# Performance work log

Measured on AMD Instinct MI355X. Metric: run time of the kernel, lower is better.

## Reference

```python
import jax, jax.numpy as jnp
import numpy as np
from jax import lax

B, C, H, W = 8, 64, 256, 256
LENGTH = 9
REDUCTION = 8
HIDDEN = max(8, C // REDUCTION)


def _conv(x, w, b, pad):
    # x: [B,Cin,H,W], w: [Cout,Cin,kh,kw]
    y = lax.conv_general_dilated(x, w, (1, 1), [(pad, pad), (pad, pad)],
                                 dimension_numbers=('NCHW', 'OIHW', 'NCHW'))
    return y + b[None, :, None, None]


def _bilinear(img, cy, cx):
    # img: [B,C,H,W]; cy,cx: [B,H,W] float coords already clipped to [0, size-1]
    # Matches F.grid_sample(mode='bilinear', padding_mode='border', align_corners=True)
    Hh, Ww = img.shape[2], img.shape[3]
    y0 = jnp.floor(cy)
    x0 = jnp.floor(cx)
    wy = (cy - y0)[:, None]  # [B,1,H,W]
    wx = (cx - x0)[:, None]
    y0i = y0.astype(jnp.int32)
    x0i = x0.astype(jnp.int32)
    y1i = jnp.minimum(y0i + 1, Hh - 1)
    x1i = jnp.minimum(x0i + 1, Ww - 1)

    def g(im, iy, ix):
        return im[:, iy, ix]  # [C,H,W]

    gather = jax.vmap(g)
    v00 = gather(img, y0i, x0i)
    v01 = gather(img, y0i, x1i)
    v10 = gather(img, y1i, x0i)
    v11 = gather(img, y1i, x1i)
    return (v00 * (1 - wy) * (1 - wx) + v01 * (1 - wy) * wx
            + v10 * wy * (1 - wx) + v11 * wy * wx)


def _oriented_pool(x, vx, vy, length):
    # x: [B,C,H,W]; vx,vy: [B,1,H,W] direction fields
    _, _, Hh, Ww = x.shape
    yy = jnp.arange(Hh, dtype=x.dtype)[None, :, None]  # [1,H,1]
    xx = jnp.arange(Ww, dtype=x.dtype)[None, None, :]  # [1,1,W]
    half = length // 2
    offsets = jnp.arange(-half, half + 1, dtype=x.dtype)
    vx2 = vx[:, 0]  # [B,H,W]
    vy2 = vy[:, 0]

    def step(acc, t):
        cy = jnp.clip(yy + t * vy2, 0.0, Hh - 1)
        cx = jnp.clip(xx + t * vx2, 0.0, Ww - 1)
        return acc + _bilinear(x, cy, cx), None

    acc, _ = lax.scan(step, jnp.zeros_like(x), offsets)
    return acc / length


def setup_inputs() -> dict:
    key = jax.random.key(0)
    ks = jax.random.split(key, 5)

    def he(k, shape, fan_in):
        return jax.random.normal(k, shape, jnp.float32) * np.float32(1.0 / np.sqrt(fan_in))

    return {
        'x': jax.random.normal(ks[0], (B, C, H, W), jnp.float32),
        'w3': he(ks[1], (HIDDEN, C, 3, 3), C * 9),
        'b3': jnp.zeros((HIDDEN,), jnp.float32),
        'w1': he(ks[2], (1, HIDDEN, 1, 1), HIDDEN),
        'b1': jnp.zeros((1,), jnp.float32),
        'wr': he(ks[3], (HIDDEN, 2 * C, 1, 1), 2 * C),
        'br': jnp.zeros((HIDDEN,), jnp.float32),
        'we': he(ks[4], (2 * C, HIDDEN, 1, 1), HIDDEN),
        'be': jnp.zeros((2 * C,), jnp.float32),
    }


def reference(x, w3, b3, w1, b1, wr, br, we, be):
    theta = jnp.pi * jax.nn.sigmoid(_conv(jax.nn.relu(_conv(x, w3, b3, 1)), w1, b1, 0))  # [B,1,H,W]
    cos_t = jnp.cos(theta)
    sin_t = jnp.sin(theta)
    tan_feat = _oriented_pool(x, cos_t, sin_t, LENGTH)
    nor_feat = _oriented_pool(x, -sin_t, cos_t, LENGTH)
    context = jnp.concatenate([tan_feat, nor_feat], axis=1)  # [B,2C,H,W]
    w = jax.nn.sigmoid(_conv(jax.nn.relu(_conv(context, wr, br, 0)), we, be, 0))  # [B,2C,H,W]
    alpha_tan, alpha_norm = jnp.split(w, 2, axis=1)
    return (alpha_tan + alpha_norm) * x
```

## Files before the change

### kernel.cpp

```cpp
#include <hip/hip_runtime.h>
#include <math.h>

#define Bb 8
#define Cc 64
#define Hh 256
#define Ww 256
#define HID 8
#define PLANE (Hh*Ww)

typedef float fvec4 __attribute__((ext_vector_type(4)));

#define TPH 13
#define TPW 74
#define TPP 75
#define TPN (TPH*TPW)

__global__ __launch_bounds__(256, 3) void fused_kernel(
    const float* __restrict__ x,
    const float* __restrict__ w3, const float* __restrict__ b3,
    const float* __restrict__ w1, const float* __restrict__ b1,
    const float* __restrict__ wr, const float* __restrict__ br,
    const float* __restrict__ we, const float* __restrict__ be,
    float* __restrict__ out)
{
    __shared__ fvec4 tile[TPH * TPP];
    const int tid = threadIdx.x;
    const int tx = tid & 63;
    const int ty = tid >> 6;
    const int xx = blockIdx.x * 64 + tx;
    const int yy = blockIdx.y * 4 + ty;
    const int b  = blockIdx.z;
    const int row0 = blockIdx.y * 4 - 4;
    const int col0 = blockIdx.x * 64 - 4;

    int goff[4], loff[4];
    #pragma unroll
    for (int k = 0; k < 4; k++) {
        int i = tid + k * 256;
        i = (i < TPN) ? i : (TPN - 1);
        const int r  = i / TPW;
        const int cc = i - r * TPW;
        const int gy = min(max(row0 + r, 0), Hh - 1);
        const int gx = min(max(col0 + cc, 0), Ww - 1);
        goff[k] = gy * Ww + gx;
        loff[k] = r * TPP + cc;
    }
    #pragma unroll
    for (int k = 0; k < 4; k++)
        asm volatile("" : "+v"(goff[k]), "+v"(loff[k]));

    const int lcen = (ty + 4) * TPP + (tx + 4);
    const float* xb = x + (size_t)b * Cc * PLANE;

    const bool interior = (blockIdx.y > 0) && (blockIdx.y < (Hh/4 - 1)) &&
                          (blockIdx.x > 0) && (blockIdx.x < (Ww/64 - 1));
    float mk[9];
    #pragma unroll
    for (int dy = 0; dy < 3; dy++)
        #pragma unroll
        for (int dx = 0; dx < 3; dx++) {
            const int gy = yy + dy - 1, gx = xx + dx - 1;
            mk[dy*3+dx] = (gy >= 0 && gy < Hh && gx >= 0 && gx < Ww) ? 1.f : 0.f;
        }

    float rv[4][4];
    #pragma unroll
    for (int k = 0; k < 4; k++)
        #pragma unroll
        for (int q = 0; q < 4; q++)
            rv[k][q] = xb[goff[k] + (size_t)q * PLANE];

    float acc[HID];
    #pragma unroll
    for (int h = 0; h < HID; h++) acc[h] = 0.f;

    for (int st = 0; st < Cc / 4; st++) {
        __syncthreads();
        #pragma unroll
        for (int k = 0; k < 4; k++)
            tile[loff[k]] = (fvec4){rv[k][0], rv[k][1], rv[k][2], rv[k][3]};
        {
            const int nst = (st + 1 < Cc / 4) ? st + 1 : 0;
            const float* xn = xb + (size_t)nst * 4 * PLANE;
            #pragma unroll
            for (int k = 0; k < 4; k++)
                #pragma unroll
                for (int q = 0; q < 4; q++)
                    rv[k][q] = xn[goff[k] + (size_t)q * PLANE];
        }
        __syncthreads();

        fvec4 va[9];
        #pragma unroll
        for (int dy = 0; dy < 3; dy++)
            #pragma unroll
            for (int dx = 0; dx < 3; dx++)
                va[dy*3+dx] = tile[lcen + (dy - 1) * TPP + (dx - 1)];
        if (!interior) {
            #pragma unroll
            for (int k = 0; k < 9; k++) va[k] *= mk[k];
        }
        #pragma unroll
        for (int h = 0; h < HID; h++) {
            const float* wk = w3 + (size_t)(h * Cc + st * 4) * 9;
            float a = acc[h];
            #pragma unroll
            for (int q = 0; q < 4; q++)
                #pragma unroll
                for (int k = 0; k < 9; k++)
                    a = fmaf(wk[q * 9 + k], va[k][q], a);
            acc[h] = a;
        }
    }

    float z = b1[0];
    #pragma unroll
    for (int h = 0; h < HID; h++) {
        float hr = acc[h] + b3[h];
        hr = hr > 0.f ? hr : 0.f;
        z = fmaf(w1[h], hr, z);
    }
    const float theta = 3.14159265358979f / (1.f + __expf(-z));
    float vy, vx;
    __sincosf(theta, &vy, &vx);

    int   off[16];
    float cw00[16], cw01[16], cw10[16], cw11[16];
    #pragma unroll
    for (int s = 0; s < 9; s++) {
        if (s == 4) continue;
        const int j = (s < 4) ? s : s - 1;
        const float t = (float)(s - 4);
        {
            float cy = fminf(fmaxf((float)yy + t * vy, 0.f), (float)(Hh - 1));
            float cx = fminf(fmaxf((float)xx + t * vx, 0.f), (float)(Ww - 1));
            int y0 = min((int)cy, Hh - 2);
            int x0 = min((int)cx, Ww - 2);
            off[j] = (y0 - row0) * TPP + (x0 - col0);
            const float wy = cy - (float)y0, wx = cx - (float)x0;
            cw00[j] = (1.f - wy) * (1.f - wx);
            cw01[j] = (1.f - wy) * wx;
            cw10[j] = wy * (1.f - wx);
            cw11[j] = wy * wx;
        }
        {
            float cy = fminf(fmaxf((float)yy + t * vx, 0.f), (float)(Hh - 1));
            float cx = fminf(fmaxf((float)xx - t * vy, 0.f), (float)(Ww - 1));
            int y0 = min((int)cy, Hh - 2);
            int x0 = min((int)cx, Ww - 2);
            off[8 + j] = (y0 - row0) * TPP + (x0 - col0);
            const float wy = cy - (float)y0, wx = cx - (float)x0;
            cw00[8 + j] = (1.f - wy) * (1.f - wx);
            cw01[8 + j] = (1.f - wy) * wx;
            cw10[8 + j] = wy * (1.f - wx);
            cw11[8 + j] = wy * wx;
        }
    }
    #pragma unroll
    for (int s = 0; s < 16; s++) {
        asm volatile("" : "+v"(off[s]), "+v"(cw00[s]), "+v"(cw01[s]));
        asm volatile("" : "+v"(cw10[s]), "+v"(cw11[s]));
    }

    float hid[HID];
    #pragma unroll
    for (int h = 0; h < HID; h++) hid[h] = br[h];

    for (int cp = 0; cp < Cc / 4; cp++) {
        __syncthreads();
        #pragma unroll
        for (int k = 0; k < 4; k++)
            tile[loff[k]] = (fvec4){rv[k][0], rv[k][1], rv[k][2], rv[k][3]};
        if (cp + 1 < Cc / 4) {
            const float* xn = xb + (size_t)(cp + 1) * 4 * PLANE;
            #pragma unroll
            for (int k = 0; k < 4; k++)
                #pragma unroll
                for (int q = 0; q < 4; q++)
                    rv[k][q] = xn[goff[k] + (size_t)q * PLANE];
        }
        __syncthreads();

        const fvec4 cent = tile[lcen];
        float tac[4], nac[4];
        #pragma unroll
        for (int q = 0; q < 4; q++) { tac[q] = cent[q]; nac[q] = cent[q]; }

        #pragma unroll
        for (int s = 0; s < 16; s++) {
            const int o = off[s];
            const fvec4 a00 = tile[o];
            const fvec4 a01 = tile[o + 1];
            const fvec4 a10 = tile[o + TPP];
            const fvec4 a11 = tile[o + TPP + 1];
            const float u00 = cw00[s], u01 = cw01[s];
            const float u10 = cw10[s], u11 = cw11[s];
            #pragma unroll
            for (int q = 0; q < 4; q++) {
                float a = (s < 8) ? tac[q] : nac[q];
                a = fmaf(a00[q], u00, a);
                a = fmaf(a01[q], u01, a);
                a = fmaf(a10[q], u10, a);
                a = fmaf(a11[q], u11, a);
                if (s < 8) tac[q] = a; else nac[q] = a;
            }
        }
        const int c = 4 * cp;
        #pragma unroll
        for (int q = 0; q < 4; q++) {
            const float tq = tac[q] * (1.f / 9.f);
            const float nq = nac[q] * (1.f / 9.f);
            #pragma unroll
            for (int h = 0; h < HID; h++) {
                float a = hid[h];
                a = fmaf(wr[h * 128 + c + q],      tq, a);
                a = fmaf(wr[h * 128 + 64 + c + q], nq, a);
                hid[h] = a;
            }
        }
    }

    #pragma unroll
    for (int h = 0; h < HID; h++) hid[h] = fmaxf(hid[h], 0.f);

    const int pix = yy * Ww + xx;
    for (int c = 0; c < Cc; c++) {
        float z1 = be[c];
        float z2 = be[c + 64];
        #pragma unroll
        for (int h = 0; h < HID; h++) {
            z1 = fmaf(we[c * 8 + h],        hid[h], z1);
            z2 = fmaf(we[(c + 64) * 8 + h], hid[h], z2);
        }
        const float a1 = 1.f / (1.f + __expf(-z1));
        const float a2 = 1.f / (1.f + __expf(-z2));
        const float xv = xb[c * PLANE + pix];
        out[(size_t)(b * Cc + c) * PLANE + pix] = (a1 + a2) * xv;
    }
}

extern "C" void kernel_launch(void* const* d_in, const int* in_sizes, int n_in,
                              void* d_out, int out_size, void* d_ws, size_t ws_size,
                              hipStream_t stream) {
    const float* x  = (const float*)d_in[0];
    const float* w3 = (const float*)d_in[1];
    const float* b3 = (const float*)d_in[2];
    const float* w1 = (const float*)d_in[3];
    const float* b1 = (const float*)d_in[4];
    const float* wr = (const float*)d_in[5];
    const float* br = (const float*)d_in[6];
    const float* we = (const float*)d_in[7];
    const float* be = (const float*)d_in[8];
    float* out = (float*)d_out;

    dim3 grid(Ww / 64, Hh / 4, Bb);
    dim3 block(256);
    fused_kernel<<<grid, block, 0, stream>>>(x, w3, b3, w1, b1,
                                             wr, br, we, be, out);
}
```

Baseline: 527.8 us.

## Store shared tile in fp16 and do bilinear lerps with packed half math

The shared-memory tile of x is converted from fp32 float4 to packed fp16 (uint2), which halves LDS footprint and gather bandwidth. The bilinear sampling now uses packed f16x2 lerps with fp16 x/y weights in place of four fp32 weight products, and occupancy hint is raised from 3 to 4 blocks per CU. This reduces LDS traffic, VALU work and register pressure, at the cost of fp16 rounding of both the input values and the interpolation weights, which may exceed the accuracy tolerance.

```diff
diff --git a/kernel.cpp b/kernel.cpp
--- a/kernel.cpp
+++ b/kernel.cpp
@@ -8,14 +8,21 @@
 #define HID 8
 #define PLANE (Hh*Ww)
 
-typedef float fvec4 __attribute__((ext_vector_type(4)));
+typedef _Float16 f16x2 __attribute__((ext_vector_type(2)));
+
+static __device__ __forceinline__ f16x2 u2h(unsigned int u) {
+    return __builtin_bit_cast(f16x2, u);
+}
+static __device__ __forceinline__ unsigned int h2u(f16x2 h) {
+    return __builtin_bit_cast(unsigned int, h);
+}
 
 #define TPH 13
 #define TPW 74
 #define TPP 75
 #define TPN (TPH*TPW)
 
-__global__ __launch_bounds__(256, 3) void fused_kernel(
+__global__ __launch_bounds__(256, 4) void fused_kernel(
     const float* __restrict__ x,
     const float* __restrict__ w3, const float* __restrict__ b3,
     const float* __restrict__ w1, const float* __restrict__ b1,
@@ -23,7 +30,7 @@
     const float* __restrict__ we, const float* __restrict__ be,
     float* __restrict__ out)
 {
-    __shared__ fvec4 tile[TPH * TPP];
+    __shared__ uint2 tile[TPH * TPP];
     const int tid = threadIdx.x;
     const int tx = tid & 63;
     const int ty = tid >> 6;
@@ -78,7 +85,9 @@
         __syncthreads();
         #pragma unroll
         for (int k = 0; k < 4; k++)
-            tile[loff[k]] = (fvec4){rv[k][0], rv[k][1], rv[k][2], rv[k][3]};
+            tile[loff[k]] = make_uint2(
+                h2u((f16x2){(_Float16)rv[k][0], (_Float16)rv[k][1]}),
+                h2u((f16x2){(_Float16)rv[k][2], (_Float16)rv[k][3]}));
         {
             const int nst = (st + 1 < Cc / 4) ? st + 1 : 0;
             const float* xn = xb + (size_t)nst * 4 * PLANE;
@@ -90,15 +99,22 @@
         }
         __syncthreads();
 
-        fvec4 va[9];
+        float va[9][4];
         #pragma unroll
         for (int dy = 0; dy < 3; dy++)
             #pragma unroll
-            for (int dx = 0; dx < 3; dx++)
-                va[dy*3+dx] = tile[lcen + (dy - 1) * TPP + (dx - 1)];
+            for (int dx = 0; dx < 3; dx++) {
+                const uint2 cv = tile[lcen + (dy - 1) * TPP + (dx - 1)];
+                const f16x2 lo = u2h(cv.x), hi = u2h(cv.y);
+                const int k = dy * 3 + dx;
+                va[k][0] = (float)lo.x; va[k][1] = (float)lo.y;
+                va[k][2] = (float)hi.x; va[k][3] = (float)hi.y;
+            }
         if (!interior) {
             #pragma unroll
-            for (int k = 0; k < 9; k++) va[k] *= mk[k];
+            for (int k = 0; k < 9; k++)
+                #pragma unroll
+                for (int q = 0; q < 4; q++) va[k][q] *= mk[k];
         }
         #pragma unroll
         for (int h = 0; h < HID; h++) {
@@ -124,8 +140,8 @@
     float vy, vx;
     __sincosf(theta, &vy, &vx);
 
-    int   off[16];
-    float cw00[16], cw01[16], cw10[16], cw11[16];
+    int off[16];
+    unsigned int wxp[16], wyp[16];
     #pragma unroll
     for (int s = 0; s < 9; s++) {
         if (s == 4) continue;
@@ -137,11 +153,9 @@
             int y0 = min((int)cy, Hh - 2);
             int x0 = min((int)cx, Ww - 2);
             off[j] = (y0 - row0) * TPP + (x0 - col0);
-            const float wy = cy - (float)y0, wx = cx - (float)x0;
-            cw00[j] = (1.f - wy) * (1.f - wx);
-            cw01[j] = (1.f - wy) * wx;
-            cw10[j] = wy * (1.f - wx);
-            cw11[j] = wy * wx;
+            const float wy = cy - (float)y0, wxx = cx - (float)x0;
+            wxp[j] = h2u((f16x2){(_Float16)wxx, (_Float16)wxx});
+            wyp[j] = h2u((f16x2){(_Float16)wy,  (_Float16)wy});
         }
         {
             float cy = fminf(fmaxf((float)yy + t * vx, 0.f), (float)(Hh - 1));
@@ -149,18 +163,14 @@
             int y0 = min((int)cy, Hh - 2);
             int x0 = min((int)cx, Ww - 2);
             off[8 + j] = (y0 - row0) * TPP + (x0 - col0);
-            const float wy = cy - (float)y0, wx = cx - (float)x0;
-            cw00[8 + j] = (1.f - wy) * (1.f - wx);
-            cw01[8 + j] = (1.f - wy) * wx;
-            cw10[8 + j] = wy * (1.f - wx);
-            cw11[8 + j] = wy * wx;
-        }
-    }
-    #pragma unroll
-    for (int s = 0; s < 16; s++) {
-        asm volatile("" : "+v"(off[s]), "+v"(cw00[s]), "+v"(cw01[s]));
-        asm volatile("" : "+v"(cw10[s]), "+v"(cw11[s]));
-    }
+            const float wy = cy - (float)y0, wxx = cx - (float)x0;
+            wxp[8 + j] = h2u((f16x2){(_Float16)wxx, (_Float16)wxx});
+            wyp[8 + j] = h2u((f16x2){(_Float16)wy,  (_Float16)wy});
+        }
+    }
+    #pragma unroll
+    for (int s = 0; s < 16; s++)
+        asm volatile("" : "+v"(off[s]), "+v"(wxp[s]), "+v"(wyp[s]));
 
     float hid[HID];
     #pragma unroll
@@ -170,7 +180,9 @@
         __syncthreads();
         #pragma unroll
         for (int k = 0; k < 4; k++)
-            tile[loff[k]] = (fvec4){rv[k][0], rv[k][1], rv[k][2], rv[k][3]};
+            tile[loff[k]] = make_uint2(
+                h2u((f16x2){(_Float16)rv[k][0], (_Float16)rv[k][1]}),
+                h2u((f16x2){(_Float16)rv[k][2], (_Float16)rv[k][3]}));
         if (cp + 1 < Cc / 4) {
             const float* xn = xb + (size_t)(cp + 1) * 4 * PLANE;
             #pragma unroll
@@ -181,29 +193,37 @@
         }
         __syncthreads();
 
-        const fvec4 cent = tile[lcen];
+        const uint2 cc = tile[lcen];
+        const f16x2 clo = u2h(cc.x), chi = u2h(cc.y);
         float tac[4], nac[4];
-        #pragma unroll
-        for (int q = 0; q < 4; q++) { tac[q] = cent[q]; nac[q] = cent[q]; }
+        tac[0] = nac[0] = (float)clo.x;
+        tac[1] = nac[1] = (float)clo.y;
+        tac[2] = nac[2] = (float)chi.x;
+        tac[3] = nac[3] = (float)chi.y;
 
         #pragma unroll
         for (int s = 0; s < 16; s++) {
             const int o = off[s];
-            const fvec4 a00 = tile[o];
-            const fvec4 a01 = tile[o + 1];
-            const fvec4 a10 = tile[o + TPP];
-            const fvec4 a11 = tile[o + TPP + 1];
-            const float u00 = cw00[s], u01 = cw01[s];
-            const float u10 = cw10[s], u11 = cw11[s];
-            #pragma unroll
-            for (int q = 0; q < 4; q++) {
-                float a = (s < 8) ? tac[q] : nac[q];
-                a = fmaf(a00[q], u00, a);
-                a = fmaf(a01[q], u01, a);
-                a = fmaf(a10[q], u10, a);
-                a = fmaf(a11[q], u11, a);
-                if (s < 8) tac[q] = a; else nac[q] = a;
-            }
+            const uint2 c00 = tile[o];
+            const uint2 c01 = tile[o + 1];
+            const uint2 c10 = tile[o + TPP];
+            const uint2 c11 = tile[o + TPP + 1];
+            const f16x2 wxh = u2h(wxp[s]);
+            const f16x2 wyh = u2h(wyp[s]);
+            const f16x2 a00 = u2h(c00.x), a01 = u2h(c01.x);
+            const f16x2 a10 = u2h(c10.x), a11 = u2h(c11.x);
+            const f16x2 e00 = u2h(c00.y), e01 = u2h(c01.y);
+            const f16x2 e10 = u2h(c10.y), e11 = u2h(c11.y);
+            const f16x2 t0  = a00 + wxh * (a01 - a00);
+            const f16x2 b0v = a10 + wxh * (a11 - a10);
+            const f16x2 t1  = e00 + wxh * (e01 - e00);
+            const f16x2 b1v = e10 + wxh * (e11 - e10);
+            const f16x2 v0  = t0 + wyh * (b0v - t0);
+            const f16x2 v1  = t1 + wyh * (b1v - t1);
+            const float s0 = (float)v0.x, s1 = (float)v0.y;
+            const float s2 = (float)v1.x, s3 = (float)v1.y;
+            if (s < 8) { tac[0]+=s0; tac[1]+=s1; tac[2]+=s2; tac[3]+=s3; }
+            else       { nac[0]+=s0; nac[1]+=s1; nac[2]+=s2; nac[3]+=s3; }
         }
         const int c = 4 * cp;
         #pragma unroll
```

Result: faster. 499.2 us (-5.4%).
